# Optimization experiments

Measured on AMD Instinct MI355X. Metric: run time of the kernel, lower is better.

## Reference

```python
import jax, jax.numpy as jnp
import numpy as np

D_MODEL = 256; D_FLOW = 128; D_FFN = 1024
N_HEADS = 8; N_LEVELS = 3; N_POINTS = 4
D_HEAD = D_MODEL // N_HEADS
SHAPES = np.array([[128, 128], [64, 64], [32, 32]], dtype=np.int64)


def setup_inputs():
    key = jax.random.key(0)
    ks = jax.random.split(key, 12)
    N = 2
    LeNin = int((SHAPES[:, 0] * SHAPES[:, 1]).sum())
    Lq = int(SHAPES[0, 0] * SHAPES[0, 1])
    lsi = np.concatenate([[0], np.cumsum(SHAPES[:, 0] * SHAPES[:, 1])[:-1]])
    s = 0.02
    return {
        'src': jax.random.normal(ks[0], (N, LeNin, D_MODEL), jnp.float32),
        'flow': jax.random.normal(ks[1], (N, Lq, D_FLOW), jnp.float32),
        'spatial_shapes': jnp.asarray(SHAPES, jnp.int32),
        'level_start_index': jnp.asarray(lsi, jnp.int32),
        'w_value': jax.random.normal(ks[2], (D_MODEL, D_MODEL), jnp.float32) * s,
        'b_value': jnp.zeros((D_MODEL,), jnp.float32),
        'w_off': jax.random.normal(ks[3], (D_FLOW, N_HEADS * N_LEVELS * N_POINTS * 2), jnp.float32) * s,
        'b_off': jax.random.normal(ks[4], (N_HEADS * N_LEVELS * N_POINTS * 2,), jnp.float32) * 0.5,
        'w_attn': jax.random.normal(ks[5], (D_FLOW, N_HEADS * N_LEVELS * N_POINTS), jnp.float32) * s,
        'b_attn': jnp.zeros((N_HEADS * N_LEVELS * N_POINTS,), jnp.float32),
        'w_out': jax.random.normal(ks[6], (D_MODEL, D_MODEL), jnp.float32) * s,
        'b_out': jnp.zeros((D_MODEL,), jnp.float32),
        'gamma': jnp.ones((D_MODEL,), jnp.float32),
        'beta': jnp.zeros((D_MODEL,), jnp.float32),
        'w1': jax.random.normal(ks[7], (D_MODEL, D_FFN), jnp.float32) * s,
        'b1': jnp.zeros((D_FFN,), jnp.float32),
        'w2': jax.random.normal(ks[8], (D_FFN, D_MODEL), jnp.float32) * s,
        'b2': jnp.zeros((D_MODEL,), jnp.float32),
    }


def _bilinear_level(v, xy, H, W):
    # v: [N, nh, H*W, dh]; xy: [N, Lq, nh, np, 2] normalized to [0,1]
    # grid_sample(align_corners=False) semantics: pixel = loc * size - 0.5, zero padding
    N, Lq = xy.shape[0], xy.shape[1]
    x = xy[..., 0] * W - 0.5
    y = xy[..., 1] * H - 0.5
    x0 = jnp.floor(x); y0 = jnp.floor(y)
    dx = x - x0; dy = y - y0
    acc = jnp.zeros((N, N_HEADS, Lq * N_POINTS, v.shape[-1]), v.dtype)
    corners = ((x0, y0, (1 - dx) * (1 - dy)),
               (x0 + 1, y0, dx * (1 - dy)),
               (x0, y0 + 1, (1 - dx) * dy),
               (x0 + 1, y0 + 1, dx * dy))
    for ix, iy, w in corners:
        valid = (ix >= 0) & (ix <= W - 1) & (iy >= 0) & (iy <= H - 1)
        xi = jnp.clip(ix, 0, W - 1).astype(jnp.int32)
        yi = jnp.clip(iy, 0, H - 1).astype(jnp.int32)
        idx = (yi * W + xi).transpose(0, 2, 1, 3).reshape(N, N_HEADS, Lq * N_POINTS)
        g = jnp.take_along_axis(v, idx[..., None], axis=2)  # [N, nh, Lq*np, dh]
        wv = (w * valid).transpose(0, 2, 1, 3).reshape(N, N_HEADS, Lq * N_POINTS, 1)
        acc = acc + wv * g
    return acc


def reference(src, flow, spatial_shapes, level_start_index, w_value, b_value,
              w_off, b_off, w_attn, b_attn, w_out, b_out, gamma, beta, w1, b1, w2, b2):
    ss = np.asarray(jax.device_get(spatial_shapes))
    lsi = np.asarray(jax.device_get(level_start_index))
    N, LeNin, _ = src.shape
    Lq = flow.shape[1]
    value = (src @ w_value + b_value).reshape(N, LeNin, N_HEADS, D_HEAD)
    off = (flow @ w_off + b_off).reshape(N, Lq, N_HEADS, N_LEVELS, N_POINTS, 2)
    attn = jax.nn.softmax((flow @ w_attn + b_attn).reshape(N, Lq, N_HEADS, N_LEVELS * N_POINTS), axis=-1)
    attn = attn.reshape(N, Lq, N_HEADS, N_LEVELS, N_POINTS)
    # reference points on level-0 grid (valid_ratios == 1)
    H0, W0 = int(ss[0, 0]), int(ss[0, 1])
    ry, rx = jnp.meshgrid(jnp.linspace(0.5, H0 - 0.5, H0) / H0,
                          jnp.linspace(0.5, W0 - 0.5, W0) / W0, indexing='ij')
    ref = jnp.stack([rx.reshape(-1), ry.reshape(-1)], -1)  # [Lq, 2] (x, y)
    norm = jnp.asarray(np.stack([ss[:, 1], ss[:, 0]], -1), jnp.float32)  # [nl, 2] = (W, H)
    loc = ref[None, :, None, None, None, :] + off / norm[None, None, None, :, None, :]
    acc = jnp.zeros((N, Lq, N_HEADS, D_HEAD), src.dtype)
    for l in range(N_LEVELS):
        H, W = int(ss[l, 0]), int(ss[l, 1])
        st = int(lsi[l])
        v = value[:, st:st + H * W].transpose(0, 2, 1, 3)  # [N, nh, HW, dh]
        s_l = _bilinear_level(v, loc[:, :, :, l], H, W).reshape(N, N_HEADS, Lq, N_POINTS, D_HEAD)
        acc = acc + jnp.einsum('bhqpd,bqhp->bqhd', s_l, attn[:, :, :, l])
    src2 = acc.reshape(N, Lq, D_MODEL) @ w_out + b_out
    x = src2  # dropout is identity at inference
    mu = x.mean(-1, keepdims=True)
    var = ((x - mu) ** 2).mean(-1, keepdims=True)
    ln = (x - mu) / jnp.sqrt(var + 1e-5) * gamma + beta
    ffn = jax.nn.relu(ln @ w1 + b1) @ w2 + b2
    return x + ffn
```

## Files before the change

### kernel.cpp

```cpp
#include <hip/hip_runtime.h>
#include <cstdint>
#include <cstddef>

#define D_MODEL  256
#define D_FLOW   128
#define D_FFN    1024
#define N_HEADS  8
#define N_LEVELS 3
#define N_POINTS 4
#define D_HEAD   32
#define LQ       16384
#define LENIN    21504
#define NB       2

typedef unsigned short ushort;
typedef __attribute__((ext_vector_type(8))) short bf16x8;
typedef __attribute__((ext_vector_type(4))) float f32x4;

__device__ __forceinline__ ushort f2b(float f) {
    uint32_t u = __float_as_uint(f);
    uint32_t r = (u + 0x7fffu + ((u >> 16) & 1u)) >> 16;
    return (ushort)r;
}

__device__ __forceinline__ void gl_lds16(const void* g, void* l) {
    __builtin_amdgcn_global_load_lds(
        (const __attribute__((address_space(1))) unsigned int*)g,
        (__attribute__((address_space(3))) unsigned int*)l,
        16, 0, 0);
}

template<bool A_FP32, bool RELU, bool RESID, bool OUT_BF16>
__global__ __launch_bounds__(256)
void mfma_gemm(const void* __restrict__ Ain, const ushort* __restrict__ Bt,
               const float* __restrict__ bias, const float* __restrict__ resid,
               void* __restrict__ Cout, int N, int K)
{
    __shared__ ushort As[128 * 64];
    __shared__ ushort Bs[128 * 64];

    const int tid  = threadIdx.x;
    const int wave = tid >> 6;
    const int lane = tid & 63;
    const int quad = lane >> 4;
    const int l16  = lane & 15;
    const int wr   = (wave >> 1) * 64;
    const int wc   = (wave & 1) * 64;
    const int bm   = blockIdx.y * 128;
    const int bn   = blockIdx.x * 128;

    const int sr  = lane >> 3;
    const int sc  = lane & 7;
    const int gch = sc ^ sr;

    f32x4 acc[4][4] = {};
    const int swz = l16 & 7;

    for (int k0 = 0; k0 < K; k0 += 64) {
        __syncthreads();
        if (A_FP32) {
            const float* Af = (const float*)Ain;
#pragma unroll
            for (int i = 0; i < 4; ++i) {
                const int row = wave * 32 + i * 8 + sr;
                const float* p = Af + (size_t)(bm + row) * K + k0 + gch * 8;
                const float4 v0 = *(const float4*)(p);
                const float4 v1 = *(const float4*)(p + 4);
                bf16x8 pk;
                pk[0] = (short)f2b(v0.x); pk[1] = (short)f2b(v0.y);
                pk[2] = (short)f2b(v0.z); pk[3] = (short)f2b(v0.w);
                pk[4] = (short)f2b(v1.x); pk[5] = (short)f2b(v1.y);
                pk[6] = (short)f2b(v1.z); pk[7] = (short)f2b(v1.w);
                *(bf16x8*)&As[(size_t)row * 64 + sc * 8] = pk;
            }
        } else {
            const ushort* Ab = (const ushort*)Ain;
#pragma unroll
            for (int i = 0; i < 4; ++i) {
                const int row = wave * 32 + i * 8;
                gl_lds16(Ab + (size_t)(bm + row + sr) * K + k0 + gch * 8,
                         As + (size_t)row * 64);
            }
        }
#pragma unroll
        for (int i = 0; i < 4; ++i) {
            const int row = wave * 32 + i * 8;
            gl_lds16(Bt + (size_t)(bn + row + sr) * K + k0 + gch * 8,
                     Bs + (size_t)row * 64);
        }
        __syncthreads();

#pragma unroll
        for (int kk = 0; kk < 2; ++kk) {
            bf16x8 af[4], bfr[4];
#pragma unroll
            for (int mi = 0; mi < 4; ++mi) {
                const int p = (kk * 4 + quad) ^ swz;
                af[mi] = *(const bf16x8*)&As[(wr + mi * 16 + l16) * 64 + p * 8];
            }
#pragma unroll
            for (int ni = 0; ni < 4; ++ni) {
                const int p = (kk * 4 + quad) ^ swz;
                bfr[ni] = *(const bf16x8*)&Bs[(wc + ni * 16 + l16) * 64 + p * 8];
            }
#pragma unroll
            for (int mi = 0; mi < 4; ++mi)
#pragma unroll
                for (int ni = 0; ni < 4; ++ni)
                    acc[mi][ni] = __builtin_amdgcn_mfma_f32_16x16x32_bf16(
                        af[mi], bfr[ni], acc[mi][ni], 0, 0, 0);
        }
    }

#pragma unroll
    for (int mi = 0; mi < 4; ++mi) {
#pragma unroll
        for (int ni = 0; ni < 4; ++ni) {
            const int col = bn + wc + ni * 16 + l16;
            const float bb = bias[col];
#pragma unroll
            for (int r = 0; r < 4; ++r) {
                const int row = bm + wr + mi * 16 + quad * 4 + r;
                const size_t idx = (size_t)row * N + col;
                float c = acc[mi][ni][r] + bb;
                if (RELU)  c = fmaxf(c, 0.f);
                if (RESID) c += resid[idx];
                if (OUT_BF16) ((ushort*)Cout)[idx] = f2b(c);
                else          ((float*)Cout)[idx]  = c;
            }
        }
    }
}

__global__ __launch_bounds__(256)
void gemm_ln_k(const ushort* __restrict__ A, const ushort* __restrict__ Bt,
               const float* __restrict__ bias, const float* __restrict__ gamma,
               const float* __restrict__ beta,
               float* __restrict__ xout, ushort* __restrict__ lnout, int K)
{
    __shared__ ushort As[64 * 32];
    __shared__ ushort Bs[256 * 32];
    __shared__ float  sS[64][33];
    __shared__ float  sS2[64][33];
    __shared__ float  sMu[64], sRi[64];

    const int tid  = threadIdx.x;
    const int wave = tid >> 6;
    const int lane = tid & 63;
    const int quad = lane >> 4;
    const int l16  = lane & 15;
    const int wr   = (wave >> 1) * 32;
    const int wc   = (wave & 1) * 128;
    const int bm   = blockIdx.x * 64;

    const int sr  = lane >> 2;
    const int sc  = lane & 3;
    const int gch = sc ^ (sr & 3);

    f32x4 acc[2][8] = {};
    const int swz = l16 & 3;

    for (int k0 = 0; k0 < K; k0 += 32) {
        __syncthreads();
        gl_lds16(A + (size_t)(bm + wave * 16 + sr) * K + k0 + gch * 8,
                 As + wave * 16 * 32);
#pragma unroll
        for (int i = 0; i < 4; ++i) {
            const int row = wave * 64 + i * 16;
            gl_lds16(Bt + (size_t)(row + sr) * K + k0 + gch * 8,
                     Bs + (size_t)row * 32);
        }
        __syncthreads();

        bf16x8 af[2], bfr[8];
#pragma unroll
        for (int mi = 0; mi < 2; ++mi)
            af[mi] = *(const bf16x8*)&As[(wr + mi * 16 + l16) * 32 + ((quad ^ swz) << 3)];
#pragma unroll
        for (int ni = 0; ni < 8; ++ni)
            bfr[ni] = *(const bf16x8*)&Bs[(wc + ni * 16 + l16) * 32 + ((quad ^ swz) << 3)];
#pragma unroll
        for (int mi = 0; mi < 2; ++mi)
#pragma unroll
            for (int ni = 0; ni < 8; ++ni)
                acc[mi][ni] = __builtin_amdgcn_mfma_f32_16x16x32_bf16(
                    af[mi], bfr[ni], acc[mi][ni], 0, 0, 0);
    }

    float bias8[8], g8[8], b8[8];
#pragma unroll
    for (int ni = 0; ni < 8; ++ni) {
        const int col = wc + ni * 16 + l16;
        bias8[ni] = bias[col];
        g8[ni]    = gamma[col];
        b8[ni]    = beta[col];
    }

#pragma unroll
    for (int mi = 0; mi < 2; ++mi)
#pragma unroll
        for (int r = 0; r < 4; ++r) {
            float s = 0.f, s2 = 0.f;
#pragma unroll
            for (int ni = 0; ni < 8; ++ni) {
                const float c = acc[mi][ni][r] + bias8[ni];
                s += c; s2 += c * c;
            }
            const int row = wr + mi * 16 + quad * 4 + r;
            sS[row][(wave & 1) * 16 + l16]  = s;
            sS2[row][(wave & 1) * 16 + l16] = s2;
        }
    __syncthreads();

    if (tid < 64) {
        float s = 0.f, s2 = 0.f;
#pragma unroll
        for (int j = 0; j < 32; ++j) { s += sS[tid][j]; s2 += sS2[tid][j]; }
        const float mu  = s * (1.f / 256.f);
        const float var = s2 * (1.f / 256.f) - mu * mu;
        sMu[tid] = mu;
        sRi[tid] = rsqrtf(var + 1e-5f);
    }
    __syncthreads();

#pragma unroll
    for (int mi = 0; mi < 2; ++mi)
#pragma unroll
        for (int r = 0; r < 4; ++r) {
            const int lrow = wr + mi * 16 + quad * 4 + r;
            const int grow = bm + lrow;
            const float mu = sMu[lrow], ri = sRi[lrow];
#pragma unroll
            for (int ni = 0; ni < 8; ++ni) {
                const int col = wc + ni * 16 + l16;
                const float c = acc[mi][ni][r] + bias8[ni];
                xout[(size_t)grow * 256 + col]  = c;
                lnout[(size_t)grow * 256 + col] = f2b((c - mu) * ri * g8[ni] + b8[ni]);
            }
        }
}

__device__ __forceinline__ void acc8(float* a, uint4 g, float w) {
    a[0] = fmaf(w, __uint_as_float(g.x << 16), a[0]);
    a[1] = fmaf(w, __uint_as_float(g.x), a[1]);
    a[2] = fmaf(w, __uint_as_float(g.y << 16), a[2]);
    a[3] = fmaf(w, __uint_as_float(g.y), a[3]);
    a[4] = fmaf(w, __uint_as_float(g.z << 16), a[4]);
    a[5] = fmaf(w, __uint_as_float(g.z), a[5]);
    a[6] = fmaf(w, __uint_as_float(g.w << 16), a[6]);
    a[7] = fmaf(w, __uint_as_float(g.w), a[7]);
}

__global__ __launch_bounds__(256)
void sample_k(const ushort* __restrict__ value, const ushort* __restrict__ projc,
              ushort* __restrict__ acc)
{
    __shared__ float sOff[8][192];
    __shared__ float sAttn[8][96];

    const int tid = threadIdx.x;
    const int bid = blockIdx.x;
    const int bq0 = (((bid & 7) << 9) | (bid >> 3)) << 3;

    for (int i = tid; i < 8 * 288; i += 256) {
        const int qw = i / 288, j = i - qw * 288;
        const float v = __uint_as_float((uint32_t)projc[(size_t)(bq0 + qw) * 384 + j] << 16);
        if (j < 192) sOff[qw][j] = v;
        else         sAttn[qw][j - 192] = v;
    }
    __syncthreads();

    if (tid < 64) {
        const int qw = tid >> 3, h = tid & 7;
        float* row = &sAttn[qw][h * 12];
        float m = row[0];
#pragma unroll
        for (int j = 1; j < 12; ++j) m = fmaxf(m, row[j]);
        float s = 0.f;
#pragma unroll
        for (int j = 0; j < 12; ++j) { const float e = __expf(row[j] - m); row[j] = e; s += e; }
        const float inv = 1.f / s;
#pragma unroll
        for (int j = 0; j < 12; ++j) row[j] *= inv;
    }
    __syncthreads();

    const int wave = tid >> 6, lane = tid & 63;
    const int qh = lane >> 5;
    const int h  = (lane >> 2) & 7;
    const int cg = lane & 3;
    const int qw = wave * 2 + qh;
    const int bq = bq0 + qw;
    const int n  = bq >> 14;
    const int q  = bq & 16383;

    const float qx = (float)(q & 127) + 0.5f;
    const float qy = (float)(q >> 7) + 0.5f;

    const int LSIc[3] = {0, 16384, 20480};

    float a[8] = {0.f, 0.f, 0.f, 0.f, 0.f, 0.f, 0.f, 0.f};
    const ushort* vbase = value + (size_t)n * LENIN * D_MODEL + h * D_HEAD + cg * 8;

#pragma unroll
    for (int l = 0; l < N_LEVELS; ++l) {
        const int   W     = 128 >> l;
        const int   SH    = 7 - l;
        const float scale = 1.f / (float)(1 << l);
        const float cx    = qx * scale - 0.5f;
        const float cy    = qy * scale - 0.5f;
        const ushort* vlev = vbase + ((size_t)LSIc[l] << 8);
#pragma unroll
        for (int p = 0; p < N_POINTS; ++p) {
            const int ob = (h * N_LEVELS + l) * (N_POINTS * 2) + p * 2;
            const float aw = sAttn[qw][h * 12 + l * 4 + p];
            const float x = cx + sOff[qw][ob];
            const float y = cy + sOff[qw][ob + 1];
            const float x0f = floorf(x), y0f = floorf(y);
            const int x0 = (int)x0f, y0 = (int)y0f;
            const float dx = x - x0f, dy = y - y0f;
            float wx1 = dx * aw, wx0 = aw - wx1;
            float wy1 = dy,      wy0 = 1.f - dy;
            if ((unsigned)x0       > (unsigned)(W - 1)) wx0 = 0.f;
            if ((unsigned)(x0 + 1) > (unsigned)(W - 1)) wx1 = 0.f;
            if ((unsigned)y0       > (unsigned)(W - 1)) wy0 = 0.f;
            if ((unsigned)(y0 + 1) > (unsigned)(W - 1)) wy1 = 0.f;
            const int xi0 = min(max(x0, 0), W - 1);
            const int xi1 = min(max(x0 + 1, 0), W - 1);
            const int yi0 = min(max(y0, 0), W - 1);
            const int yi1 = min(max(y0 + 1, 0), W - 1);
            const uint4 g00 = *(const uint4*)(vlev + ((size_t)((yi0 << SH) + xi0) << 8));
            const uint4 g01 = *(const uint4*)(vlev + ((size_t)((yi0 << SH) + xi1) << 8));
            const uint4 g10 = *(const uint4*)(vlev + ((size_t)((yi1 << SH) + xi0) << 8));
            const uint4 g11 = *(const uint4*)(vlev + ((size_t)((yi1 << SH) + xi1) << 8));
            acc8(a, g00, wx0 * wy0);
            acc8(a, g01, wx1 * wy0);
            acc8(a, g10, wx0 * wy1);
            acc8(a, g11, wx1 * wy1);
        }
    }

    const uint32_t o0 = (uint32_t)f2b(a[0]) | ((uint32_t)f2b(a[1]) << 16);
    const uint32_t o1 = (uint32_t)f2b(a[2]) | ((uint32_t)f2b(a[3]) << 16);
    const uint32_t o2 = (uint32_t)f2b(a[4]) | ((uint32_t)f2b(a[5]) << 16);
    const uint32_t o3 = (uint32_t)f2b(a[6]) | ((uint32_t)f2b(a[7]) << 16);
    const uint4 ov = {o0, o1, o2, o3};
    *(uint4*)(acc + (size_t)bq * D_MODEL + h * D_HEAD + cg * 8) = ov;
}

__global__ __launch_bounds__(256)
void prep_all_k(const float* __restrict__ w_value, const float* __restrict__ w_out,
                const float* __restrict__ w1, const float* __restrict__ w2,
                const float* __restrict__ w_off, const float* __restrict__ b_off,
                const float* __restrict__ w_attn, const float* __restrict__ b_attn,
                ushort* __restrict__ wvT, ushort* __restrict__ woT,
                ushort* __restrict__ w1T, ushort* __restrict__ w2T,
                ushort* __restrict__ wcT, float* __restrict__ biasc)
{
    int i = blockIdx.x * 256 + threadIdx.x;
    if (i < 65536) {
        const int k = i >> 8, n = i & 255;
        wvT[(size_t)n * 256 + k] = f2b(w_value[i]);
        return;
    }
    i -= 65536;
    if (i < 65536) {
        const int k = i >> 8, n = i & 255;
        woT[(size_t)n * 256 + k] = f2b(w_out[i]);
        return;
    }
    i -= 65536;
    if (i < 262144) {
        const int k = i >> 10, n = i & 1023;
        w1T[(size_t)n * 256 + k] = f2b(w1[i]);
        return;
    }
    i -= 262144;
    if (i < 262144) {
        const int k = i >> 8, n = i & 255;
        w2T[(size_t)n * 1024 + k] = f2b(w2[i]);
        return;
    }
    i -= 262144;
    if (i < 49152) {
        const int nn = i >> 7, k = i & 127;
        float v = 0.f;
        if (nn < 192)      v = w_off[(size_t)k * 192 + nn];
        else if (nn < 288) v = w_attn[(size_t)k * 96 + (nn - 192)];
        wcT[i] = f2b(v);
        return;
    }
    i -= 49152;
    if (i < 384) {
        float b = 0.f;
        if (i < 192)      b = b_off[i];
        else if (i < 288) b = b_attn[i - 192];
        biasc[i] = b;
    }
}

extern "C" void kernel_launch(void* const* d_in, const int* in_sizes, int n_in,
                              void* d_out, int out_size, void* d_ws, size_t ws_size,
                              hipStream_t stream)
{
    const float* src     = (const float*)d_in[0];
    const float* flow    = (const float*)d_in[1];
    const float* w_value = (const float*)d_in[4];
    const float* b_value = (const float*)d_in[5];
    const float* w_off   = (const float*)d_in[6];
    const float* b_off   = (const float*)d_in[7];
    const float* w_attn  = (const float*)d_in[8];
    const float* b_attn  = (const float*)d_in[9];
    const float* w_out   = (const float*)d_in[10];
    const float* b_out   = (const float*)d_in[11];
    const float* gamma   = (const float*)d_in[12];
    const float* beta    = (const float*)d_in[13];
    const float* w1      = (const float*)d_in[14];
    const float* b1      = (const float*)d_in[15];
    const float* w2      = (const float*)d_in[16];
    const float* b2      = (const float*)d_in[17];
    float* out = (float*)d_out;
    char*  wsb = (char*)d_ws;

    ushort* ffn1_bf  = (ushort*)(wsb);
    ushort* value_bf = (ushort*)(wsb);
    ushort* acc_bf   = (ushort*)(wsb + 22020096);
    ushort* projc_bf = (ushort*)(wsb + 67108864);
    ushort* ln_bf    = (ushort*)(wsb + 67108864);
    ushort* wvT      = (ushort*)(wsb + 92274688);
    ushort* woT      = (ushort*)(wsb + 92405760);
    ushort* w1T      = (ushort*)(wsb + 92536832);
    ushort* w2T      = (ushort*)(wsb + 93061120);
    ushort* wcT      = (ushort*)(wsb + 93585408);
    float*  biasc    = (float*) (wsb + 93683712);

    const int Mq = NB * LQ;
    const int Mv = NB * LENIN;

    prep_all_k<<<2754, 256, 0, stream>>>(w_value, w_out, w1, w2,
                                         w_off, b_off, w_attn, b_attn,
                                         wvT, woT, w1T, w2T, wcT, biasc);

    mfma_gemm<true, false, false, true><<<dim3(2, Mv / 128), 256, 0, stream>>>(
        src, wvT, b_value, nullptr, value_bf, 256, 256);

    mfma_gemm<true, false, false, true><<<dim3(3, Mq / 128), 256, 0, stream>>>(
        flow, wcT, biasc, nullptr, projc_bf, 384, 128);

    sample_k<<<Mq / 8, 256, 0, stream>>>(value_bf, projc_bf, acc_bf);

    gemm_ln_k<<<Mq / 64, 256, 0, stream>>>(
        acc_bf, woT, b_out, gamma, beta, out, ln_bf, 256);

    mfma_gemm<false, true, false, true><<<dim3(8, Mq / 128), 256, 0, stream>>>(
        ln_bf, w1T, b1, nullptr, ffn1_bf, 1024, 256);

    mfma_gemm<false, false, true, false><<<dim3(2, Mq / 128), 256, 0, stream>>>(
        ffn1_bf, w2T, b2, out, out, 256, 1024);
}
```

Baseline: 293.4 us.

## Fuse FFN up and down projections into one kernel, swizzle GEMM block order

Replaces the two FFN GEMM launches with a single fused kernel. It computes a 64-row tile of the hidden activation in 32-column chunks, keeps each chunk in shared memory, and immediately accumulates it into the down-projection, with double-buffered W1 loads. This avoids writing and re-reading the 32768x1024 bf16 intermediate in global memory. W2 is repacked into chunk-contiguous layout in the prep kernel. Generic GEMM blocks are also remapped by a linear swizzle to change L2 locality, at the cost of more syncs per chunk and lower occupancy risk from 512-thread blocks.

```diff
diff --git a/kernel.cpp b/kernel.cpp
--- a/kernel.cpp
+++ b/kernel.cpp
@@ -46,8 +46,15 @@
     const int l16  = lane & 15;
     const int wr   = (wave >> 1) * 64;
     const int wc   = (wave & 1) * 64;
-    const int bm   = blockIdx.y * 128;
-    const int bn   = blockIdx.x * 128;
+
+    const int nx = gridDim.x;
+    int lin = blockIdx.y * nx + blockIdx.x;
+    const int total = nx * gridDim.y;
+    if ((total & 7) == 0) lin = (lin & 7) * (total >> 3) + (lin >> 3);
+    const int by = lin / nx;
+    const int bx = lin - by * nx;
+    const int bm = by * 128;
+    const int bn = bx * 128;
 
     const int sr  = lane >> 3;
     const int sc  = lane & 7;
@@ -238,6 +245,140 @@
                 lnout[(size_t)grow * 256 + col] = f2b((c - mu) * ri * g8[ni] + b8[ni]);
             }
         }
+}
+
+__global__ __launch_bounds__(512, 3)
+void ffn_fused_k(const ushort* __restrict__ ln, const ushort* __restrict__ w1T,
+                 const ushort* __restrict__ w2C, const float* __restrict__ b1v,
+                 const float* __restrict__ b2v, float* __restrict__ out)
+{
+    __shared__ ushort smem[29696];
+    ushort* const w1s0 = smem;
+    ushort* const w1s1 = smem + 8192;
+    ushort* const w2s  = smem + 16384;
+    ushort* const hS0  = smem + 24576;
+    ushort* const hS1  = smem + 27136;
+    ushort* const lnS  = smem + 8192;
+
+    const int tid  = threadIdx.x;
+    const int wave = tid >> 6;
+    const int lane = tid & 63;
+    const int quad = lane >> 4;
+    const int l16  = lane & 15;
+    const int g1m  = wave >> 1;
+    const int g1n  = wave & 1;
+    const int wm   = wave >> 2;
+    const int wn   = wave & 3;
+    const int bm   = blockIdx.x * 64;
+
+    const int sr2  = lane >> 5, sc32 = lane & 31;
+    const int sr4  = lane >> 2, sc4  = lane & 3;
+
+#pragma unroll
+    for (int i = 0; i < 4; ++i) {
+        const int r0 = (wave * 4 + i) * 2;
+        const int r  = r0 + sr2;
+        gl_lds16(ln + (size_t)(bm + r) * 256 + ((sc32 ^ (r & 7)) << 3),
+                 lnS + r0 * 256);
+    }
+#pragma unroll
+    for (int i = 0; i < 2; ++i) {
+        const int r0 = (wave * 2 + i) * 2;
+        const int r  = r0 + sr2;
+        gl_lds16(w1T + (size_t)r * 256 + ((sc32 ^ (r & 7)) << 3),
+                 w1s0 + r0 * 256);
+    }
+    __syncthreads();
+
+    bf16x8 afA[8];
+#pragma unroll
+    for (int kk = 0; kk < 8; ++kk)
+        afA[kk] = *(const bf16x8*)&lnS[(g1m * 16 + l16) * 256
+                                        + (((kk * 4 + quad) ^ (l16 & 7)) << 3)];
+    __syncthreads();
+
+    f32x4 acc2[2][4] = {};
+
+#pragma unroll 1
+    for (int c = 0; c < 32; ++c) {
+        ushort* const w1cur = (c & 1) ? w1s1 : w1s0;
+        ushort* const w1nxt = (c & 1) ? w1s0 : w1s1;
+        ushort* const hcur  = (c & 1) ? hS1  : hS0;
+
+        if (c < 31) {
+#pragma unroll
+            for (int i = 0; i < 2; ++i) {
+                const int r0 = (wave * 2 + i) * 2;
+                const int r  = r0 + sr2;
+                gl_lds16(w1T + (size_t)((c + 1) * 32 + r) * 256
+                             + ((sc32 ^ (r & 7)) << 3),
+                         w1nxt + r0 * 256);
+            }
+        }
+        {
+            const ushort* w2c = w2C + (size_t)c * 8192;
+#pragma unroll
+            for (int i = 0; i < 2; ++i) {
+                const int n0 = (wave * 2 + i) * 16;
+                const int rw = n0 + sr4;
+                gl_lds16(w2c + (size_t)rw * 32 + ((sc4 ^ ((rw >> 1) & 3)) << 3),
+                         w2s + n0 * 32);
+            }
+        }
+
+        f32x4 acc1 = {};
+#pragma unroll
+        for (int kk = 0; kk < 8; ++kk) {
+            const bf16x8 bf = *(const bf16x8*)&w1cur[(g1n * 16 + l16) * 256
+                                   + (((kk * 4 + quad) ^ (l16 & 7)) << 3)];
+            acc1 = __builtin_amdgcn_mfma_f32_16x16x32_bf16(afA[kk], bf, acc1, 0, 0, 0);
+        }
+
+        {
+            const int kc = g1n * 16 + l16;
+            const float bb = b1v[c * 32 + kc];
+            const int hr = g1m * 16 + quad * 4;
+#pragma unroll
+            for (int r = 0; r < 4; ++r)
+                hcur[(hr + r) * 40 + kc] = f2b(fmaxf(acc1[r] + bb, 0.f));
+        }
+        __syncthreads();
+
+        {
+            bf16x8 a2[2], b2f[4];
+#pragma unroll
+            for (int mi = 0; mi < 2; ++mi)
+                a2[mi] = *(const bf16x8*)&hcur[(wm * 32 + mi * 16 + l16) * 40
+                                               + (quad << 3)];
+#pragma unroll
+            for (int ni = 0; ni < 4; ++ni) {
+                const int row = wn * 64 + ni * 16 + l16;
+                b2f[ni] = *(const bf16x8*)&w2s[row * 32
+                              + ((quad ^ ((l16 >> 1) & 3)) << 3)];
+            }
+#pragma unroll
+            for (int mi = 0; mi < 2; ++mi)
+#pragma unroll
+                for (int ni = 0; ni < 4; ++ni)
+                    acc2[mi][ni] = __builtin_amdgcn_mfma_f32_16x16x32_bf16(
+                        a2[mi], b2f[ni], acc2[mi][ni], 0, 0, 0);
+        }
+        __syncthreads();
+    }
+
+#pragma unroll
+    for (int ni = 0; ni < 4; ++ni) {
+        const int col = wn * 64 + ni * 16 + l16;
+        const float bb = b2v[col];
+#pragma unroll
+        for (int mi = 0; mi < 2; ++mi)
+#pragma unroll
+            for (int r = 0; r < 4; ++r) {
+                const int row = bm + wm * 32 + mi * 16 + quad * 4 + r;
+                const size_t idx = (size_t)row * 256 + col;
+                out[idx] = out[idx] + acc2[mi][ni][r] + bb;
+            }
+    }
 }
 
 __device__ __forceinline__ void acc8(float* a, uint4 g, float w) {
@@ -354,7 +495,7 @@
                 const float* __restrict__ w_off, const float* __restrict__ b_off,
                 const float* __restrict__ w_attn, const float* __restrict__ b_attn,
                 ushort* __restrict__ wvT, ushort* __restrict__ woT,
-                ushort* __restrict__ w1T, ushort* __restrict__ w2T,
+                ushort* __restrict__ w1T, ushort* __restrict__ w2C,
                 ushort* __restrict__ wcT, float* __restrict__ biasc)
 {
     int i = blockIdx.x * 256 + threadIdx.x;
@@ -378,7 +519,7 @@
     i -= 262144;
     if (i < 262144) {
         const int k = i >> 8, n = i & 255;
-        w2T[(size_t)n * 1024 + k] = f2b(w2[i]);
+        w2C[(size_t)(k >> 5) * 8192 + n * 32 + (k & 31)] = f2b(w2[i]);
         return;
     }
     i -= 262144;
@@ -422,7 +563,6 @@
     float* out = (float*)d_out;
     char*  wsb = (char*)d_ws;
 
-    ushort* ffn1_bf  = (ushort*)(wsb);
     ushort* value_bf = (ushort*)(wsb);
     ushort* acc_bf   = (ushort*)(wsb + 22020096);
     ushort* projc_bf = (ushort*)(wsb + 67108864);
@@ -430,7 +570,7 @@
     ushort* wvT      = (ushort*)(wsb + 92274688);
     ushort* woT      = (ushort*)(wsb + 92405760);
     ushort* w1T      = (ushort*)(wsb + 92536832);
-    ushort* w2T      = (ushort*)(wsb + 93061120);
+    ushort* w2C      = (ushort*)(wsb + 93061120);
     ushort* wcT      = (ushort*)(wsb + 93585408);
     float*  biasc    = (float*) (wsb + 93683712);
 
@@ -439,7 +579,7 @@
 
     prep_all_k<<<2754, 256, 0, stream>>>(w_value, w_out, w1, w2,
                                          w_off, b_off, w_attn, b_attn,
-                                         wvT, woT, w1T, w2T, wcT, biasc);
+                                         wvT, woT, w1T, w2C, wcT, biasc);
 
     mfma_gemm<true, false, false, true><<<dim3(2, Mv / 128), 256, 0, stream>>>(
         src, wvT, b_value, nullptr, value_bf, 256, 256);
@@ -452,9 +592,5 @@
     gemm_ln_k<<<Mq / 64, 256, 0, stream>>>(
         acc_bf, woT, b_out, gamma, beta, out, ln_bf, 256);
 
-    mfma_gemm<false, true, false, true><<<dim3(8, Mq / 128), 256, 0, stream>>>(
-        ln_bf, w1T, b1, nullptr, ffn1_bf, 1024, 256);
-
-    mfma_gemm<false, false, true, false><<<dim3(2, Mq / 128), 256, 0, stream>>>(
-        ffn1_bf, w2T, b2, out, out, 256, 1024);
-}
+    ffn_fused_k<<<Mq / 64, 512, 0, stream>>>(ln_bf, w1T, w2C, b1, b2, out);
+}
```

After: 270.6 us. 7.8% less time.

## Fuse FFN up and down projections into one kernel and swizzle GEMM block order

Applied to the files above, without the earlier changes.

Replaces the two FFN GEMM launches with a single kernel. Each 128-row block computes the ReLU hidden activations in 64-column chunks into shared memory and immediately accumulates them into the down-projection, so the 32768x1024 bf16 hidden tensor never round-trips through global memory. W2 is re-laid out into per-chunk tiles in the prep kernel to match. The generic GEMM also remaps block indices so consecutive blocks are interleaved, aiming at better cache locality. The fused kernel launches only 256 blocks and uses a large 80KB LDS footprint, which limits occupancy and parallelism.

```diff
diff --git a/kernel.cpp b/kernel.cpp
--- a/kernel.cpp
+++ b/kernel.cpp
@@ -46,8 +46,15 @@
     const int l16  = lane & 15;
     const int wr   = (wave >> 1) * 64;
     const int wc   = (wave & 1) * 64;
-    const int bm   = blockIdx.y * 128;
-    const int bn   = blockIdx.x * 128;
+
+    const int nx = gridDim.x;
+    int lin = blockIdx.y * nx + blockIdx.x;
+    const int total = nx * gridDim.y;
+    if ((total & 7) == 0) lin = (lin & 7) * (total >> 3) + (lin >> 3);
+    const int by = lin / nx;
+    const int bx = lin - by * nx;
+    const int bm = by * 128;
+    const int bn = bx * 128;
 
     const int sr  = lane >> 3;
     const int sc  = lane & 7;
@@ -238,6 +245,166 @@
                 lnout[(size_t)grow * 256 + col] = f2b((c - mu) * ri * g8[ni] + b8[ni]);
             }
         }
+}
+
+__global__ __launch_bounds__(512, 2)
+void ffn_fused_k(const ushort* __restrict__ ln, const ushort* __restrict__ w1T,
+                 const ushort* __restrict__ w2C, const float* __restrict__ b1v,
+                 const float* __restrict__ b2v, float* __restrict__ out)
+{
+    extern __shared__ ushort smem[];
+    ushort* const w1s = smem;
+    ushort* const w2s = smem + 16384;
+    ushort* const hS  = smem + 32768;
+    ushort* const lnS = smem;
+
+    const int tid  = threadIdx.x;
+    const int wave = tid >> 6;
+    const int lane = tid & 63;
+    const int quad = lane >> 4;
+    const int l16  = lane & 15;
+    const int bm   = blockIdx.x * 128;
+
+    const int R0g1 = (wave >> 1) * 32;
+    const int C0g1 = (wave & 1) * 32;
+    const int M0   = (wave & 1) * 64;
+    const int N0   = (wave >> 1) * 64;
+
+#pragma unroll
+    for (int i = 0; i < 8; ++i) {
+        const int r0 = (wave * 8 + i) * 2;
+        const int r  = r0 + (lane >> 5);
+        gl_lds16(ln + (size_t)(bm + r) * 256 + (((lane & 31) ^ (r & 7)) << 3),
+                 lnS + r0 * 256);
+    }
+    __syncthreads();
+
+    bf16x8 afA[2][8];
+#pragma unroll
+    for (int mt = 0; mt < 2; ++mt)
+#pragma unroll
+        for (int kk = 0; kk < 8; ++kk) {
+            const int row = R0g1 + mt * 16 + l16;
+            afA[mt][kk] = *(const bf16x8*)
+                &lnS[row * 256 + (((kk * 4 + quad) ^ (row & 7)) << 3)];
+        }
+    __syncthreads();
+
+#pragma unroll
+    for (int i = 0; i < 4; ++i) {
+        const int r0 = (wave * 4 + i) * 2;
+        const int r  = r0 + (lane >> 5);
+        gl_lds16(w1T + (size_t)r * 256 + (((lane & 31) ^ (r & 7)) << 3),
+                 w1s + r0 * 256);
+    }
+    __syncthreads();
+
+    f32x4 acc2[4][4] = {};
+
+#pragma unroll 1
+    for (int c = 0; c < 16; ++c) {
+        {
+            const ushort* src = w2C + (size_t)c * 16384;
+#pragma unroll
+            for (int i = 0; i < 4; ++i) {
+                const int r0 = (wave * 4 + i) * 8;
+                const int r  = r0 + (lane >> 3);
+                gl_lds16(src + (size_t)r * 64 + (((lane & 7) ^ (r & 7)) << 3),
+                         w2s + r0 * 64);
+            }
+        }
+
+        f32x4 acc1[2][2] = {};
+#pragma unroll
+        for (int kk = 0; kk < 8; ++kk) {
+            bf16x8 wf[2];
+#pragma unroll
+            for (int nt = 0; nt < 2; ++nt) {
+                const int n = C0g1 + nt * 16 + l16;
+                wf[nt] = *(const bf16x8*)
+                    &w1s[n * 256 + (((kk * 4 + quad) ^ (n & 7)) << 3)];
+            }
+#pragma unroll
+            for (int mt = 0; mt < 2; ++mt)
+#pragma unroll
+                for (int nt = 0; nt < 2; ++nt)
+                    acc1[mt][nt] = __builtin_amdgcn_mfma_f32_16x16x32_bf16(
+                        wf[nt], afA[mt][kk], acc1[mt][nt], 0, 0, 0);
+        }
+
+        {
+            float4 bb[2];
+#pragma unroll
+            for (int nt = 0; nt < 2; ++nt)
+                bb[nt] = *(const float4*)&b1v[c * 64 + C0g1 + nt * 16 + quad * 4];
+#pragma unroll
+            for (int mt = 0; mt < 2; ++mt) {
+                const int m = R0g1 + mt * 16 + l16;
+#pragma unroll
+                for (int nt = 0; nt < 2; ++nt) {
+                    const int oct = (C0g1 >> 2) + nt * 4 + quad;
+                    ushort4 pk;
+                    pk.x = f2b(fmaxf(acc1[mt][nt][0] + bb[nt].x, 0.f));
+                    pk.y = f2b(fmaxf(acc1[mt][nt][1] + bb[nt].y, 0.f));
+                    pk.z = f2b(fmaxf(acc1[mt][nt][2] + bb[nt].z, 0.f));
+                    pk.w = f2b(fmaxf(acc1[mt][nt][3] + bb[nt].w, 0.f));
+                    *(ushort4*)&hS[m * 64 + ((oct ^ ((m & 7) << 1)) << 2)] = pk;
+                }
+            }
+        }
+        __syncthreads();
+
+        if (c < 15) {
+#pragma unroll
+            for (int i = 0; i < 4; ++i) {
+                const int r0 = (wave * 4 + i) * 2;
+                const int r  = r0 + (lane >> 5);
+                gl_lds16(w1T + (size_t)((c + 1) * 64 + r) * 256
+                             + (((lane & 31) ^ (r & 7)) << 3),
+                         w1s + r0 * 256);
+            }
+        }
+
+#pragma unroll
+        for (int kk = 0; kk < 2; ++kk) {
+            const int g = kk * 4 + quad;
+            bf16x8 hf[4], wf2[4];
+#pragma unroll
+            for (int mt = 0; mt < 4; ++mt) {
+                const int m = M0 + mt * 16 + l16;
+                hf[mt] = *(const bf16x8*)&hS[m * 64 + ((g ^ (m & 7)) << 3)];
+            }
+#pragma unroll
+            for (int nt = 0; nt < 4; ++nt) {
+                const int n = N0 + nt * 16 + l16;
+                wf2[nt] = *(const bf16x8*)&w2s[n * 64 + ((g ^ (n & 7)) << 3)];
+            }
+#pragma unroll
+            for (int mt = 0; mt < 4; ++mt)
+#pragma unroll
+                for (int nt = 0; nt < 4; ++nt)
+                    acc2[mt][nt] = __builtin_amdgcn_mfma_f32_16x16x32_bf16(
+                        wf2[nt], hf[mt], acc2[mt][nt], 0, 0, 0);
+        }
+        __syncthreads();
+    }
+
+#pragma unroll
+    for (int mt = 0; mt < 4; ++mt) {
+        const int row = bm + M0 + mt * 16 + l16;
+#pragma unroll
+        for (int nt = 0; nt < 4; ++nt) {
+            const int col = N0 + nt * 16 + quad * 4;
+            float4* p = (float4*)(out + (size_t)row * 256 + col);
+            const float4 b4 = *(const float4*)&b2v[col];
+            float4 v = *p;
+            v.x = v.x + acc2[mt][nt][0] + b4.x;
+            v.y = v.y + acc2[mt][nt][1] + b4.y;
+            v.z = v.z + acc2[mt][nt][2] + b4.z;
+            v.w = v.w + acc2[mt][nt][3] + b4.w;
+            *p = v;
+        }
+    }
 }
 
 __device__ __forceinline__ void acc8(float* a, uint4 g, float w) {
@@ -354,7 +521,7 @@
                 const float* __restrict__ w_off, const float* __restrict__ b_off,
                 const float* __restrict__ w_attn, const float* __restrict__ b_attn,
                 ushort* __restrict__ wvT, ushort* __restrict__ woT,
-                ushort* __restrict__ w1T, ushort* __restrict__ w2T,
+                ushort* __restrict__ w1T, ushort* __restrict__ w2C,
                 ushort* __restrict__ wcT, float* __restrict__ biasc)
 {
     int i = blockIdx.x * 256 + threadIdx.x;
@@ -378,7 +545,7 @@
     i -= 262144;
     if (i < 262144) {
         const int k = i >> 8, n = i & 255;
-        w2T[(size_t)n * 1024 + k] = f2b(w2[i]);
+        w2C[(size_t)(k >> 6) * 16384 + n * 64 + (k & 63)] = f2b(w2[i]);
         return;
     }
     i -= 262144;
@@ -422,7 +589,6 @@
     float* out = (float*)d_out;
     char*  wsb = (char*)d_ws;
 
-    ushort* ffn1_bf  = (ushort*)(wsb);
     ushort* value_bf = (ushort*)(wsb);
     ushort* acc_bf   = (ushort*)(wsb + 22020096);
     ushort* projc_bf = (ushort*)(wsb + 67108864);
@@ -430,16 +596,23 @@
     ushort* wvT      = (ushort*)(wsb + 92274688);
     ushort* woT      = (ushort*)(wsb + 92405760);
     ushort* w1T      = (ushort*)(wsb + 92536832);
-    ushort* w2T      = (ushort*)(wsb + 93061120);
+    ushort* w2C      = (ushort*)(wsb + 93061120);
     ushort* wcT      = (ushort*)(wsb + 93585408);
     float*  biasc    = (float*) (wsb + 93683712);
 
     const int Mq = NB * LQ;
     const int Mv = NB * LENIN;
 
+    static bool ffn_attr_done = false;
+    if (!ffn_attr_done) {
+        hipFuncSetAttribute((const void*)ffn_fused_k,
+                            hipFuncAttributeMaxDynamicSharedMemorySize, 81920);
+        ffn_attr_done = true;
+    }
+
     prep_all_k<<<2754, 256, 0, stream>>>(w_value, w_out, w1, w2,
                                          w_off, b_off, w_attn, b_attn,
-                                         wvT, woT, w1T, w2T, wcT, biasc);
+                                         wvT, woT, w1T, w2C, wcT, biasc);
 
     mfma_gemm<true, false, false, true><<<dim3(2, Mv / 128), 256, 0, stream>>>(
         src, wvT, b_value, nullptr, value_bf, 256, 256);
@@ -452,9 +625,5 @@
     gemm_ln_k<<<Mq / 64, 256, 0, stream>>>(
         acc_bf, woT, b_out, gamma, beta, out, ln_bf, 256);
 
-    mfma_gemm<false, true, false, true><<<dim3(8, Mq / 128), 256, 0, stream>>>(
-        ln_bf, w1T, b1, nullptr, ffn1_bf, 1024, 256);
-
-    mfma_gemm<false, false, true, false><<<dim3(2, Mq / 128), 256, 0, stream>>>(
-        ffn1_bf, w2T, b2, out, out, 256, 1024);
-}
+    ffn_fused_k<<<Mq / 128, 512, 81920, stream>>>(ln_bf, w1T, w2C, b1, b2, out);
+}
```

Result: faster. 268.7 us (-8.4%).
